# Performance work log

Measured on AMD Instinct MI355X. Metric: run time of the kernel, lower is better.

## Reference

```python
import jax, jax.numpy as jnp
import numpy as np

D_MODEL = 1024
H = 16
D_K = D_MODEL // H  # 64
B = 4
NQ = 1024
NK = 1024


def setup_inputs() -> dict:
    key = jax.random.key(0)
    ks = jax.random.split(key, 16)
    inp = {
        "queries": jax.random.normal(ks[0], (B, NQ, D_MODEL), jnp.float32),
        "keys": jax.random.normal(ks[1], (B, NK, D_MODEL), jnp.float32),
        "values": jax.random.normal(ks[2], (B, NK, D_MODEL), jnp.float32),
        "attention_weights": jax.random.uniform(ks[3], (B, H, NQ, NK), jnp.float32),
        "attention_mask": jax.random.randint(ks[4], (B, H, NQ, NK), 0, 2).astype(bool),
        # Linear params, init.normal_(std=0.001), zero bias (torch Linear: y = x @ W.T + b)
        "Wq": 0.001 * jax.random.normal(ks[5], (D_MODEL, D_MODEL), jnp.float32),
        "bq": jnp.zeros((D_MODEL,), jnp.float32),
        "Wk": 0.001 * jax.random.normal(ks[6], (D_MODEL, D_MODEL), jnp.float32),
        "bk": jnp.zeros((D_MODEL,), jnp.float32),
        "Wv": 0.001 * jax.random.normal(ks[7], (D_MODEL, D_MODEL), jnp.float32),
        "bv": jnp.zeros((D_MODEL,), jnp.float32),
        "Wo": 0.001 * jax.random.normal(ks[8], (D_MODEL, D_MODEL), jnp.float32),
        "bo": jnp.zeros((D_MODEL,), jnp.float32),
    }
    return inp


def reference(queries, keys, values, attention_weights, attention_mask,
              Wq, bq, Wk, bk, Wv, bv, Wo, bo):
    b_s, nq, _ = queries.shape
    nk = keys.shape[1]
    # projections -> (b, h, n, d_k)
    q = (queries @ Wq.T + bq).reshape(b_s, nq, H, D_K).transpose(0, 2, 1, 3)
    k = (keys @ Wk.T + bk).reshape(b_s, nk, H, D_K).transpose(0, 2, 1, 3)
    v = (values @ Wv.T + bv).reshape(b_s, nk, H, D_K).transpose(0, 2, 1, 3)
    scale = 1.0 / np.sqrt(D_K).astype(np.float32)
    att = jnp.einsum("bhqd,bhkd->bhqk", q, k) * scale
    att = att * attention_weights
    att = jnp.where(attention_mask, -jnp.inf, att)
    att = jax.nn.softmax(att, axis=-1)
    # dropout is identity in eval mode
    out = jnp.einsum("bhqk,bhkd->bhqd", att, v)
    out = out.transpose(0, 2, 1, 3).reshape(b_s, nq, H * D_K)
    out = out @ Wo.T + bo
    return (out, att)
```

## Files before the change

### kernel.cpp

```cpp
#include <hip/hip_runtime.h>
#include <stdint.h>

#define B_ 4
#define H_ 16
#define NQ_ 1024
#define NK_ 1024
#define DM_ 1024
#define DK_ 64

typedef __attribute__((ext_vector_type(8))) short short8;
typedef __attribute__((ext_vector_type(4))) float f32x4;
typedef unsigned short u16;
typedef unsigned int u32;

__device__ __forceinline__ u16 f2bf(float f) {
  u32 u = __builtin_bit_cast(u32, f);
  u32 r = u + 0x7fffu + ((u >> 16) & 1u);
  return (u16)(r >> 16);
}

__device__ __forceinline__ float bf2f(u16 b) {
  u32 u = ((u32)b) << 16;
  return __builtin_bit_cast(float, u);
}

__device__ __forceinline__ short8 ld_short8(const u16* p) {
  return __builtin_bit_cast(short8, *(const int4*)p);
}

__device__ __forceinline__ int4 gload16(const void* p) {
  int4 d;
  asm volatile("global_load_dwordx4 %0, %1, off" : "=v"(d) : "v"(p));
  return d;
}
__device__ __forceinline__ int2 gload8(const void* p) {
  int2 d;
  asm volatile("global_load_dwordx2 %0, %1, off" : "=v"(d) : "v"(p));
  return d;
}
#define VMW(N) do { asm volatile("s_waitcnt vmcnt(" #N ")" ::: "memory"); \
                    __builtin_amdgcn_sched_barrier(0); } while (0)

__global__ void detect_mask_kernel(const unsigned char* __restrict__ m, int* __restrict__ flag) {
  if (threadIdx.x == 0) {
    int f = 0;
    for (int i = 0; i < 256; ++i)
      if ((i & 3) != 0 && m[i] != 0) f = 1;
    *flag = f;
  }
}

__global__ __launch_bounds__(256) void gemm_kernel(
    const float* __restrict__ Aq, const float* __restrict__ Ak, const float* __restrict__ Av,
    const u16* __restrict__ Ao,
    const float* __restrict__ Wq, const float* __restrict__ Wk,
    const float* __restrict__ Wv, const float* __restrict__ Wo,
    const float* __restrict__ bq, const float* __restrict__ bk,
    const float* __restrict__ bv, const float* __restrict__ bo,
    u16* __restrict__ qbuf, u16* __restrict__ kbuf, u16* __restrict__ vTbuf,
    float* __restrict__ outbuf, int mode_base)
{
  const int z = mode_base + (int)blockIdx.z;
  const int n0 = blockIdx.x * 128;
  const int m0 = blockIdx.y * 128;
  const int tid = threadIdx.x;
  const int lane = tid & 63;
  const int wave = tid >> 6;
  const int wm = wave >> 1, wn = wave & 1;

  __shared__ u16 Al[128 * 40];
  __shared__ u16 Bl[128 * 40];

  const float* Af = (z == 0) ? Aq : (z == 1 ? Ak : Av);
  const float* W  = (z == 0) ? Wq : (z == 1 ? Wk : (z == 2 ? Wv : Wo));

  f32x4 acc[4][4];
#pragma unroll
  for (int i = 0; i < 4; ++i)
#pragma unroll
    for (int j = 0; j < 4; ++j) acc[i][j] = (f32x4){0.f, 0.f, 0.f, 0.f};

  float4 arf[4];
  int4   arb[2];
  float4 brf[4];

  auto load_tiles = [&](int ks) {
    const int kk0 = ks * 32;
    if (z < 3) {
#pragma unroll
      for (int c = 0; c < 4; ++c) {
        int chunk = c * 256 + tid;
        arf[c] = *(const float4*)(Af + (size_t)(m0 + (chunk >> 3)) * DM_ + kk0 + (chunk & 7) * 4);
      }
    } else {
#pragma unroll
      for (int c = 0; c < 2; ++c) {
        int chunk = c * 256 + tid;
        arb[c] = *(const int4*)(Ao + (size_t)(m0 + (chunk >> 2)) * DM_ + kk0 + (chunk & 3) * 8);
      }
    }
#pragma unroll
    for (int c = 0; c < 4; ++c) {
      int chunk = c * 256 + tid;
      brf[c] = *(const float4*)(W + (size_t)(n0 + (chunk >> 3)) * DM_ + kk0 + (chunk & 7) * 4);
    }
  };

  auto store_lds = [&]() {
    if (z < 3) {
#pragma unroll
      for (int c = 0; c < 4; ++c) {
        int chunk = c * 256 + tid;
        ushort4 p;
        p.x = f2bf(arf[c].x); p.y = f2bf(arf[c].y); p.z = f2bf(arf[c].z); p.w = f2bf(arf[c].w);
        *(ushort4*)(Al + (chunk >> 3) * 40 + (chunk & 7) * 4) = p;
      }
    } else {
#pragma unroll
      for (int c = 0; c < 2; ++c) {
        int chunk = c * 256 + tid;
        *(int4*)(Al + (chunk >> 2) * 40 + (chunk & 3) * 8) = arb[c];
      }
    }
#pragma unroll
    for (int c = 0; c < 4; ++c) {
      int chunk = c * 256 + tid;
      ushort4 p;
      p.x = f2bf(brf[c].x); p.y = f2bf(brf[c].y); p.z = f2bf(brf[c].z); p.w = f2bf(brf[c].w);
      *(ushort4*)(Bl + (chunk >> 3) * 40 + (chunk & 7) * 4) = p;
    }
  };

  load_tiles(0);
  for (int ks = 0; ks < 32; ++ks) {
    __syncthreads();
    store_lds();
    __syncthreads();
    if (ks < 31) load_tiles(ks + 1);
    short8 afr[4], bfr[4];
#pragma unroll
    for (int i = 0; i < 4; ++i) {
      afr[i] = ld_short8(Al + (wm * 64 + i * 16 + (lane & 15)) * 40 + (lane >> 4) * 8);
      bfr[i] = ld_short8(Bl + (wn * 64 + i * 16 + (lane & 15)) * 40 + (lane >> 4) * 8);
    }
#pragma unroll
    for (int i = 0; i < 4; ++i)
#pragma unroll
      for (int j = 0; j < 4; ++j)
        acc[i][j] = __builtin_amdgcn_mfma_f32_16x16x32_bf16(afr[i], bfr[j], acc[i][j], 0, 0, 0);
  }

  const float* bias = (z == 0) ? bq : (z == 1 ? bk : (z == 2 ? bv : bo));
#pragma unroll
  for (int i = 0; i < 4; ++i) {
    const int token0 = m0 + wm * 64 + i * 16 + (lane >> 4) * 4;
#pragma unroll
    for (int j = 0; j < 4; ++j) {
      const int feat = n0 + wn * 64 + j * 16 + (lane & 15);
      const float bvl = bias[feat];
      if (z == 3) {
#pragma unroll
        for (int r = 0; r < 4; ++r)
          outbuf[(size_t)(token0 + r) * DM_ + feat] = acc[i][j][r] + bvl;
      } else if (z == 2) {
        const int bb = token0 >> 10, t = token0 & 1023;
        const int hh = feat >> 6, d = feat & 63;
        ushort4 p;
        p.x = f2bf(acc[i][j][0] + bvl);
        p.y = f2bf(acc[i][j][1] + bvl);
        p.z = f2bf(acc[i][j][2] + bvl);
        p.w = f2bf(acc[i][j][3] + bvl);
        *(ushort4*)(vTbuf + ((size_t)(bb * H_ + hh) * DK_ + d) * NK_ + t) = p;
      } else {
        u16* dst = (z == 0) ? qbuf : kbuf;
        const int hh = feat >> 6, d = feat & 63;
#pragma unroll
        for (int r = 0; r < 4; ++r) {
          const int token = token0 + r;
          const int bb = token >> 10, t = token & 1023;
          dst[((size_t)(bb * H_ + hh) * NQ_ + t) * DK_ + d] = f2bf(acc[i][j][r] + bvl);
        }
      }
    }
  }
}

__global__ __launch_bounds__(512) void attn_kernel(
    const u16* __restrict__ qbuf, const u16* __restrict__ kbuf, const u16* __restrict__ vTbuf,
    const float* __restrict__ aw, const void* __restrict__ maskp, const int* __restrict__ flagp,
    float* __restrict__ attout, u16* __restrict__ obuf)
{
  __shared__ u16 S[16 * 1024];

  const int n = blockIdx.x;
  const int work = (n & 7) * 512 + (n >> 3);
  const int qt = work & 63;
  const int bh = work >> 6;
  const int b = bh >> 4, h = bh & 15;
  const int qbase = qt * 16;
  const int tid = threadIdx.x;
  const int lane = tid & 63;
  const int wave = tid >> 6;
  const int hi = lane >> 4;
  const int l15 = lane & 15;
  const int mflag = *flagp;

  {
    const u16* qp = qbuf + ((size_t)bh * NQ_ + qbase + l15) * DK_ + hi * 8;
    int4 qd0 = gload16(qp);
    int4 qd1 = gload16(qp + 32);

    const u16* kbase = kbuf + (size_t)bh * NK_ * DK_;
    const int tkc = wave * 16 + l15;
    int4 kq0[8], kq1[8];

#define QK_ISSUE(t) do { \
    const u16* kp_ = kbase + (size_t)((t) * 128 + tkc) * DK_ + hi * 8; \
    kq0[t] = gload16(kp_); \
    kq1[t] = gload16(kp_ + 32); } while (0)

    QK_ISSUE(0); QK_ISSUE(1); QK_ISSUE(2); QK_ISSUE(3);
    VMW(4);
    const short8 qf0 = __builtin_bit_cast(short8, qd0);
    const short8 qf1 = __builtin_bit_cast(short8, qd1);

#define QK_EAT(t) do { \
    f32x4 sacc_ = (f32x4){0.f, 0.f, 0.f, 0.f}; \
    sacc_ = __builtin_amdgcn_mfma_f32_16x16x32_bf16(qf0, __builtin_bit_cast(short8, kq0[t]), sacc_, 0, 0, 0); \
    sacc_ = __builtin_amdgcn_mfma_f32_16x16x32_bf16(qf1, __builtin_bit_cast(short8, kq1[t]), sacc_, 0, 0, 0); \
    const int tk_ = (t) * 128 + tkc; \
    _Pragma("unroll") \
    for (int r = 0; r < 4; ++r) { \
      const int row_ = hi * 4 + r; \
      S[row_ * 1024 + (tk_ ^ ((row_ & 7) << 3))] = f2bf(sacc_[r]); \
    } } while (0)

    QK_EAT(0); QK_EAT(1);
    QK_ISSUE(4); QK_ISSUE(5);
    VMW(4);
    QK_EAT(2); QK_EAT(3);
    QK_ISSUE(6); QK_ISSUE(7);
    VMW(4);
    QK_EAT(4); QK_EAT(5);
    VMW(0);
    QK_EAT(6); QK_EAT(7);
#undef QK_ISSUE
#undef QK_EAT
  }
  __syncthreads();

  {
    const int c0 = lane * 8;
    const float scale = 0.125f;
    const size_t ab0 = ((size_t)bh * NQ_ + qbase + wave) * (size_t)NK_;
    const size_t ab1 = ab0 + 8 * (size_t)NK_;

#define SM_CONSUME(row_, bm_, A0_, A1_, A2_, A3_, ab_) do { \
    u16* Srow_ = S + (row_) * 1024; \
    const int swz_ = ((row_) & 7) << 3; \
    const short8 sL_ = ld_short8(Srow_ + (c0 ^ swz_)); \
    const short8 sH_ = ld_short8(Srow_ + ((c0 + 512) ^ swz_)); \
    const f32x4 awA_ = __builtin_bit_cast(f32x4, A0_); \
    const f32x4 awB_ = __builtin_bit_cast(f32x4, A1_); \
    const f32x4 awC_ = __builtin_bit_cast(f32x4, A2_); \
    const f32x4 awD_ = __builtin_bit_cast(f32x4, A3_); \
    f32x4 eA_, eB_, eC_, eD_; \
    _Pragma("unroll") \
    for (int jj = 0; jj < 4; ++jj) { \
      eA_[jj] = (((bm_) >> jj) & 1u) ? 0.f : __expf(bf2f((u16)sL_[jj]) * scale * awA_[jj]); \
      eB_[jj] = (((bm_) >> (4 + jj)) & 1u) ? 0.f : __expf(bf2f((u16)sL_[4 + jj]) * scale * awB_[jj]); \
      eC_[jj] = (((bm_) >> (8 + jj)) & 1u) ? 0.f : __expf(bf2f((u16)sH_[jj]) * scale * awC_[jj]); \
      eD_[jj] = (((bm_) >> (12 + jj)) & 1u) ? 0.f : __expf(bf2f((u16)sH_[4 + jj]) * scale * awD_[jj]); \
    } \
    float sum_ = 0.f; \
    _Pragma("unroll") \
    for (int jj = 0; jj < 4; ++jj) sum_ += (eA_[jj] + eB_[jj]) + (eC_[jj] + eD_[jj]); \
    _Pragma("unroll") \
    for (int o_ = 32; o_ >= 1; o_ >>= 1) sum_ += __shfl_xor(sum_, o_); \
    const float inv_ = 1.0f / sum_; \
    eA_ *= inv_; eB_ *= inv_; eC_ *= inv_; eD_ *= inv_; \
    *(f32x4*)(attout + (ab_) + c0) = eA_; \
    *(f32x4*)(attout + (ab_) + c0 + 4) = eB_; \
    *(f32x4*)(attout + (ab_) + c0 + 512) = eC_; \
    *(f32x4*)(attout + (ab_) + c0 + 516) = eD_; \
    short8 pL_, pH_; \
    _Pragma("unroll") \
    for (int jj = 0; jj < 4; ++jj) { \
      pL_[jj] = (short)f2bf(eA_[jj]); pL_[4 + jj] = (short)f2bf(eB_[jj]); \
      pH_[jj] = (short)f2bf(eC_[jj]); pH_[4 + jj] = (short)f2bf(eD_[jj]); \
    } \
    *(int4*)(Srow_ + (c0 ^ swz_)) = __builtin_bit_cast(int4, pL_); \
    *(int4*)(Srow_ + ((c0 + 512) ^ swz_)) = __builtin_bit_cast(int4, pH_); \
  } while (0)

    if (mflag) {
      const unsigned char* mp = (const unsigned char*)maskp;
      int4 a00 = gload16(aw + ab0 + c0);
      int4 a01 = gload16(aw + ab0 + c0 + 4);
      int4 a02 = gload16(aw + ab0 + c0 + 512);
      int4 a03 = gload16(aw + ab0 + c0 + 516);
      int2 m00 = gload8(mp + ab0 + c0);
      int2 m01 = gload8(mp + ab0 + c0 + 512);
      int4 a10 = gload16(aw + ab1 + c0);
      int4 a11 = gload16(aw + ab1 + c0 + 4);
      int4 a12 = gload16(aw + ab1 + c0 + 512);
      int4 a13 = gload16(aw + ab1 + c0 + 516);
      int2 m10 = gload8(mp + ab1 + c0);
      int2 m11 = gload8(mp + ab1 + c0 + 512);
      VMW(6);
      u32 bm0 = 0;
#pragma unroll
      for (int j = 0; j < 4; ++j) {
        bm0 |= (((u32)m00.x >> (8 * j)) & 1u) << j;
        bm0 |= (((u32)m00.y >> (8 * j)) & 1u) << (4 + j);
        bm0 |= (((u32)m01.x >> (8 * j)) & 1u) << (8 + j);
        bm0 |= (((u32)m01.y >> (8 * j)) & 1u) << (12 + j);
      }
      SM_CONSUME(wave, bm0, a00, a01, a02, a03, ab0);
      VMW(0);
      u32 bm1 = 0;
#pragma unroll
      for (int j = 0; j < 4; ++j) {
        bm1 |= (((u32)m10.x >> (8 * j)) & 1u) << j;
        bm1 |= (((u32)m10.y >> (8 * j)) & 1u) << (4 + j);
        bm1 |= (((u32)m11.x >> (8 * j)) & 1u) << (8 + j);
        bm1 |= (((u32)m11.y >> (8 * j)) & 1u) << (12 + j);
      }
      SM_CONSUME(wave + 8, bm1, a10, a11, a12, a13, ab1);
    } else {
      const int* mp = (const int*)maskp;
      int4 a00 = gload16(aw + ab0 + c0);
      int4 a01 = gload16(aw + ab0 + c0 + 4);
      int4 a02 = gload16(aw + ab0 + c0 + 512);
      int4 a03 = gload16(aw + ab0 + c0 + 516);
      int4 m00 = gload16(mp + ab0 + c0);
      int4 m01 = gload16(mp + ab0 + c0 + 4);
      int4 m02 = gload16(mp + ab0 + c0 + 512);
      int4 m03 = gload16(mp + ab0 + c0 + 516);
      int4 a10 = gload16(aw + ab1 + c0);
      int4 a11 = gload16(aw + ab1 + c0 + 4);
      int4 a12 = gload16(aw + ab1 + c0 + 512);
      int4 a13 = gload16(aw + ab1 + c0 + 516);
      int4 m10 = gload16(mp + ab1 + c0);
      int4 m11 = gload16(mp + ab1 + c0 + 4);
      int4 m12 = gload16(mp + ab1 + c0 + 512);
      int4 m13 = gload16(mp + ab1 + c0 + 516);
      VMW(8);
      u32 bm0 = ((u32)m00.x) | ((u32)m00.y << 1) | ((u32)m00.z << 2) | ((u32)m00.w << 3)
              | ((u32)m01.x << 4) | ((u32)m01.y << 5) | ((u32)m01.z << 6) | ((u32)m01.w << 7)
              | ((u32)m02.x << 8) | ((u32)m02.y << 9) | ((u32)m02.z << 10) | ((u32)m02.w << 11)
              | ((u32)m03.x << 12) | ((u32)m03.y << 13) | ((u32)m03.z << 14) | ((u32)m03.w << 15);
      SM_CONSUME(wave, bm0, a00, a01, a02, a03, ab0);
      VMW(0);
      u32 bm1 = ((u32)m10.x) | ((u32)m10.y << 1) | ((u32)m10.z << 2) | ((u32)m10.w << 3)
              | ((u32)m11.x << 4) | ((u32)m11.y << 5) | ((u32)m11.z << 6) | ((u32)m11.w << 7)
              | ((u32)m12.x << 8) | ((u32)m12.y << 9) | ((u32)m12.z << 10) | ((u32)m12.w << 11)
              | ((u32)m13.x << 12) | ((u32)m13.y << 13) | ((u32)m13.z << 14) | ((u32)m13.w << 15);
      SM_CONSUME(wave + 8, bm1, a10, a11, a12, a13, ab1);
    }
#undef SM_CONSUME
  }
  __syncthreads();

  {
    const int kh = wave >> 2;
    const int j = wave & 3;
    const u16* Sr = S + l15 * 1024;
    const int asw = (l15 & 7) << 3;
    const int dcol = j * 16 + l15;
    const u16* vb = vTbuf + ((size_t)bh * DK_ + dcol) * (size_t)NK_;
    const int kh512 = kh * 512;
    f32x4 o0 = (f32x4){0.f, 0.f, 0.f, 0.f};
    f32x4 o1 = (f32x4){0.f, 0.f, 0.f, 0.f};
    int4 vq[16];

#define PV_ISSUE(t) do { vq[t] = gload16(vb + kh512 + (t) * 32 + hi * 8); } while (0)
#define PV_EAT(t) do { \
    const int c_ = kh512 + (t) * 32 + hi * 8; \
    const short8 pa_ = ld_short8(Sr + (c_ ^ asw)); \
    if ((t) & 1) o1 = __builtin_amdgcn_mfma_f32_16x16x32_bf16(pa_, __builtin_bit_cast(short8, vq[t]), o1, 0, 0, 0); \
    else        o0 = __builtin_amdgcn_mfma_f32_16x16x32_bf16(pa_, __builtin_bit_cast(short8, vq[t]), o0, 0, 0, 0); \
  } while (0)

    PV_ISSUE(0); PV_ISSUE(1); PV_ISSUE(2); PV_ISSUE(3);
    PV_ISSUE(4); PV_ISSUE(5); PV_ISSUE(6); PV_ISSUE(7);
    VMW(4);
    PV_EAT(0); PV_EAT(1); PV_EAT(2); PV_EAT(3);
    PV_ISSUE(8); PV_ISSUE(9); PV_ISSUE(10); PV_ISSUE(11);
    VMW(4);
    PV_EAT(4); PV_EAT(5); PV_EAT(6); PV_EAT(7);
    PV_ISSUE(12); PV_ISSUE(13); PV_ISSUE(14); PV_ISSUE(15);
    VMW(4);
    PV_EAT(8); PV_EAT(9); PV_EAT(10); PV_EAT(11);
    VMW(0);
    PV_EAT(12); PV_EAT(13); PV_EAT(14); PV_EAT(15);
#undef PV_ISSUE
#undef PV_EAT

    f32x4 oacc = o0 + o1;
    __syncthreads();
    float* Pbuf = (float*)S;
    if (kh == 1) {
#pragma unroll
      for (int r = 0; r < 4; ++r)
        Pbuf[(hi * 4 + r) * 64 + dcol] = oacc[r];
    }
    __syncthreads();
    if (kh == 0) {
      const int feat = h * DK_ + dcol;
#pragma unroll
      for (int r = 0; r < 4; ++r) {
        const int row = hi * 4 + r;
        obuf[((size_t)b * NQ_ + qbase + row) * DM_ + feat] =
            f2bf(oacc[r] + Pbuf[row * 64 + dcol]);
      }
    }
  }
}

extern "C" void kernel_launch(void* const* d_in, const int* in_sizes, int n_in,
                              void* d_out, int out_size, void* d_ws, size_t ws_size,
                              hipStream_t stream)
{
  const float* queries = (const float*)d_in[0];
  const float* keys    = (const float*)d_in[1];
  const float* values  = (const float*)d_in[2];
  const float* aw      = (const float*)d_in[3];
  const void*  maskp   = d_in[4];
  const float* Wq = (const float*)d_in[5];
  const float* bq = (const float*)d_in[6];
  const float* Wk = (const float*)d_in[7];
  const float* bk = (const float*)d_in[8];
  const float* Wv = (const float*)d_in[9];
  const float* bv = (const float*)d_in[10];
  const float* Wo = (const float*)d_in[11];
  const float* bo = (const float*)d_in[12];

  char* ws = (char*)d_ws;
  const size_t NE = (size_t)B_ * H_ * NQ_ * DK_;
  int* flag  = (int*)ws;
  u16* qbuf  = (u16*)(ws + 256);
  u16* kbuf  = qbuf + NE;
  u16* vTbuf = kbuf + NE;
  u16* obuf  = vTbuf + NE;
  if (ws_size < 256 + 8 * NE) return;

  float* outp = (float*)d_out;
  float* attp = outp + (size_t)B_ * NQ_ * DM_;

  detect_mask_kernel<<<1, 64, 0, stream>>>((const unsigned char*)maskp, flag);

  gemm_kernel<<<dim3(8, 32, 3), 256, 0, stream>>>(queries, keys, values, obuf,
      Wq, Wk, Wv, Wo, bq, bk, bv, bo, qbuf, kbuf, vTbuf, outp, 0);

  attn_kernel<<<dim3(4096), 512, 0, stream>>>(qbuf, kbuf, vTbuf, aw, maskp, flag,
                                              attp, obuf);

  gemm_kernel<<<dim3(8, 32, 1), 256, 0, stream>>>(queries, keys, values, obuf,
      Wq, Wk, Wv, Wo, bq, bk, bv, bo, qbuf, kbuf, vTbuf, outp, 3);
}
```

Before: 354.0 us.

## Split fused attention kernel into separate QK-softmax and PV kernels

Splits the fused attention kernel into two kernels. The first computes the scores, applies weights and mask, runs the softmax and writes the attention matrix. The second re-reads that fp32 attention matrix from global memory, converts it to bf16 and runs the P·V MFMA with 256-thread blocks. This drops the shared-memory staging and the intra-block split-K reduction, and it lowers register and LDS pressure in the first kernel. The cost is a full extra read of the large attention matrix from global memory plus an additional kernel launch.

Result: slower. 473.0 us (+33.6%).

```diff
diff --git a/kernel.cpp b/kernel.cpp
--- a/kernel.cpp
+++ b/kernel.cpp
@@ -185,10 +185,10 @@
   }
 }
 
-__global__ __launch_bounds__(512) void attn_kernel(
-    const u16* __restrict__ qbuf, const u16* __restrict__ kbuf, const u16* __restrict__ vTbuf,
+__global__ __launch_bounds__(512) void qk_softmax_kernel(
+    const u16* __restrict__ qbuf, const u16* __restrict__ kbuf,
     const float* __restrict__ aw, const void* __restrict__ maskp, const int* __restrict__ flagp,
-    float* __restrict__ attout, u16* __restrict__ obuf)
+    float* __restrict__ attout)
 {
   __shared__ u16 S[16 * 1024];
 
@@ -196,7 +196,6 @@
   const int work = (n & 7) * 512 + (n >> 3);
   const int qt = work & 63;
   const int bh = work >> 6;
-  const int b = bh >> 4, h = bh & 15;
   const int qbase = qt * 16;
   const int tid = threadIdx.x;
   const int lane = tid & 63;
@@ -283,14 +282,6 @@
     *(f32x4*)(attout + (ab_) + c0 + 4) = eB_; \
     *(f32x4*)(attout + (ab_) + c0 + 512) = eC_; \
     *(f32x4*)(attout + (ab_) + c0 + 516) = eD_; \
-    short8 pL_, pH_; \
-    _Pragma("unroll") \
-    for (int jj = 0; jj < 4; ++jj) { \
-      pL_[jj] = (short)f2bf(eA_[jj]); pL_[4 + jj] = (short)f2bf(eB_[jj]); \
-      pH_[jj] = (short)f2bf(eC_[jj]); pH_[4 + jj] = (short)f2bf(eD_[jj]); \
-    } \
-    *(int4*)(Srow_ + (c0 ^ swz_)) = __builtin_bit_cast(int4, pL_); \
-    *(int4*)(Srow_ + ((c0 + 512) ^ swz_)) = __builtin_bit_cast(int4, pH_); \
   } while (0)
 
     if (mflag) {
@@ -360,61 +351,77 @@
     }
 #undef SM_CONSUME
   }
-  __syncthreads();
-
-  {
-    const int kh = wave >> 2;
-    const int j = wave & 3;
-    const u16* Sr = S + l15 * 1024;
-    const int asw = (l15 & 7) << 3;
-    const int dcol = j * 16 + l15;
-    const u16* vb = vTbuf + ((size_t)bh * DK_ + dcol) * (size_t)NK_;
-    const int kh512 = kh * 512;
-    f32x4 o0 = (f32x4){0.f, 0.f, 0.f, 0.f};
-    f32x4 o1 = (f32x4){0.f, 0.f, 0.f, 0.f};
-    int4 vq[16];
-
-#define PV_ISSUE(t) do { vq[t] = gload16(vb + kh512 + (t) * 32 + hi * 8); } while (0)
-#define PV_EAT(t) do { \
-    const int c_ = kh512 + (t) * 32 + hi * 8; \
-    const short8 pa_ = ld_short8(Sr + (c_ ^ asw)); \
-    if ((t) & 1) o1 = __builtin_amdgcn_mfma_f32_16x16x32_bf16(pa_, __builtin_bit_cast(short8, vq[t]), o1, 0, 0, 0); \
-    else        o0 = __builtin_amdgcn_mfma_f32_16x16x32_bf16(pa_, __builtin_bit_cast(short8, vq[t]), o0, 0, 0, 0); \
-  } while (0)
-
-    PV_ISSUE(0); PV_ISSUE(1); PV_ISSUE(2); PV_ISSUE(3);
-    PV_ISSUE(4); PV_ISSUE(5); PV_ISSUE(6); PV_ISSUE(7);
-    VMW(4);
-    PV_EAT(0); PV_EAT(1); PV_EAT(2); PV_EAT(3);
-    PV_ISSUE(8); PV_ISSUE(9); PV_ISSUE(10); PV_ISSUE(11);
-    VMW(4);
-    PV_EAT(4); PV_EAT(5); PV_EAT(6); PV_EAT(7);
-    PV_ISSUE(12); PV_ISSUE(13); PV_ISSUE(14); PV_ISSUE(15);
-    VMW(4);
-    PV_EAT(8); PV_EAT(9); PV_EAT(10); PV_EAT(11);
-    VMW(0);
-    PV_EAT(12); PV_EAT(13); PV_EAT(14); PV_EAT(15);
-#undef PV_ISSUE
-#undef PV_EAT
-
-    f32x4 oacc = o0 + o1;
-    __syncthreads();
-    float* Pbuf = (float*)S;
-    if (kh == 1) {
-#pragma unroll
-      for (int r = 0; r < 4; ++r)
-        Pbuf[(hi * 4 + r) * 64 + dcol] = oacc[r];
-    }
-    __syncthreads();
-    if (kh == 0) {
-      const int feat = h * DK_ + dcol;
-#pragma unroll
-      for (int r = 0; r < 4; ++r) {
-        const int row = hi * 4 + r;
-        obuf[((size_t)b * NQ_ + qbase + row) * DM_ + feat] =
-            f2bf(oacc[r] + Pbuf[row * 64 + dcol]);
-      }
-    }
+}
+
+__global__ __launch_bounds__(256) void pv_kernel(
+    const float* __restrict__ att, const u16* __restrict__ vTbuf, u16* __restrict__ obuf)
+{
+  const int n = blockIdx.x;
+  const int work = (n & 7) * 512 + (n >> 3);
+  const int qt = work & 63;
+  const int bh = work >> 6;
+  const int b = bh >> 4, h = bh & 15;
+  const int qbase = qt * 16;
+  const int tid = threadIdx.x;
+  const int lane = tid & 63;
+  const int wave = tid >> 6;
+  const int hi = lane >> 4;
+  const int l15 = lane & 15;
+
+  const float* arow = att + ((size_t)bh * NQ_ + qbase + l15) * (size_t)NK_;
+  const int dcol = wave * 16 + l15;
+  const u16* vb = vTbuf + ((size_t)bh * DK_ + dcol) * (size_t)NK_;
+
+  f32x4 o0 = (f32x4){0.f, 0.f, 0.f, 0.f};
+  f32x4 o1 = (f32x4){0.f, 0.f, 0.f, 0.f};
+  int4 pq0[8], pq1[8], vq[8];
+
+#define PB_ISSUE(t) do { const int c_ = (t) * 32 + hi * 8; \
+    pq0[(t) & 7] = gload16(arow + c_); \
+    pq1[(t) & 7] = gload16(arow + c_ + 4); \
+    vq[(t) & 7]  = gload16(vb + c_); } while (0)
+#define PB_EAT(t) do { \
+    const f32x4 f0_ = __builtin_bit_cast(f32x4, pq0[(t) & 7]); \
+    const f32x4 f1_ = __builtin_bit_cast(f32x4, pq1[(t) & 7]); \
+    short8 pa_; \
+    _Pragma("unroll") \
+    for (int jj = 0; jj < 4; ++jj) { pa_[jj] = (short)f2bf(f0_[jj]); pa_[4 + jj] = (short)f2bf(f1_[jj]); } \
+    const short8 vf_ = __builtin_bit_cast(short8, vq[(t) & 7]); \
+    if ((t) & 1) o1 = __builtin_amdgcn_mfma_f32_16x16x32_bf16(pa_, vf_, o1, 0, 0, 0); \
+    else         o0 = __builtin_amdgcn_mfma_f32_16x16x32_bf16(pa_, vf_, o0, 0, 0, 0); } while (0)
+
+  PB_ISSUE(0); PB_ISSUE(1); PB_ISSUE(2); PB_ISSUE(3);
+  PB_ISSUE(4); PB_ISSUE(5); PB_ISSUE(6); PB_ISSUE(7);
+  VMW(12);
+  PB_EAT(0); PB_EAT(1); PB_EAT(2); PB_EAT(3);
+  PB_ISSUE(8); PB_ISSUE(9); PB_ISSUE(10); PB_ISSUE(11);
+  VMW(12);
+  PB_EAT(4); PB_EAT(5); PB_EAT(6); PB_EAT(7);
+  PB_ISSUE(12); PB_ISSUE(13); PB_ISSUE(14); PB_ISSUE(15);
+  VMW(12);
+  PB_EAT(8); PB_EAT(9); PB_EAT(10); PB_EAT(11);
+  PB_ISSUE(16); PB_ISSUE(17); PB_ISSUE(18); PB_ISSUE(19);
+  VMW(12);
+  PB_EAT(12); PB_EAT(13); PB_EAT(14); PB_EAT(15);
+  PB_ISSUE(20); PB_ISSUE(21); PB_ISSUE(22); PB_ISSUE(23);
+  VMW(12);
+  PB_EAT(16); PB_EAT(17); PB_EAT(18); PB_EAT(19);
+  PB_ISSUE(24); PB_ISSUE(25); PB_ISSUE(26); PB_ISSUE(27);
+  VMW(12);
+  PB_EAT(20); PB_EAT(21); PB_EAT(22); PB_EAT(23);
+  PB_ISSUE(28); PB_ISSUE(29); PB_ISSUE(30); PB_ISSUE(31);
+  VMW(12);
+  PB_EAT(24); PB_EAT(25); PB_EAT(26); PB_EAT(27);
+  VMW(0);
+  PB_EAT(28); PB_EAT(29); PB_EAT(30); PB_EAT(31);
+#undef PB_ISSUE
+#undef PB_EAT
+
+  const int feat = h * DK_ + dcol;
+#pragma unroll
+  for (int r = 0; r < 4; ++r) {
+    const int q = qbase + hi * 4 + r;
+    obuf[((size_t)b * NQ_ + q) * DM_ + feat] = f2bf(o0[r] + o1[r]);
   }
 }
 
@@ -453,8 +460,9 @@
   gemm_kernel<<<dim3(8, 32, 3), 256, 0, stream>>>(queries, keys, values, obuf,
       Wq, Wk, Wv, Wo, bq, bk, bv, bo, qbuf, kbuf, vTbuf, outp, 0);
 
-  attn_kernel<<<dim3(4096), 512, 0, stream>>>(qbuf, kbuf, vTbuf, aw, maskp, flag,
-                                              attp, obuf);
+  qk_softmax_kernel<<<dim3(4096), 512, 0, stream>>>(qbuf, kbuf, aw, maskp, flag, attp);
+
+  pv_kernel<<<dim3(4096), 256, 0, stream>>>(attp, vTbuf, obuf);
 
   gemm_kernel<<<dim3(8, 32, 1), 256, 0, stream>>>(queries, keys, values, obuf,
       Wq, Wk, Wv, Wo, bq, bk, bv, bo, qbuf, kbuf, vTbuf, outp, 3);
```
